# Optimization experiments

Hardware: AMD Instinct MI355X
Metric: run time of the kernel (lower is better)

Reference implementation:

```python
import jax, jax.numpy as jnp
import numpy as np

N_NODES = 25000
N_EDGES = 400000
N_GRAPHS = 100
D_IN = 16
D = 32          # node_dim
K = 11          # spectral coefficients = edge_dim
NOUT1 = 30
NOUT2 = 2
L = 2           # n_interactions
D_OUT = 32


def setup_inputs() -> dict:
    key = jax.random.key(0)
    ks = jax.random.split(key, 24)
    s = 0.1
    inp = {
        'x': jax.random.normal(ks[0], (N_NODES, D_IN), jnp.float32),
        'edge_attr': jax.random.uniform(ks[1], (N_EDGES, K), jnp.float32),
        'edge_index': jax.random.randint(ks[2], (2, N_EDGES), 0, N_NODES),
        'batch': jnp.sort(jax.random.randint(ks[3], (N_NODES,), 0, N_GRAPHS)),
        # embedding
        'emb_w': jax.random.normal(ks[4], (D_IN, D)) * s,
        'emb_b': jnp.zeros((D,)),
        # per-interaction params, stacked on leading L axis
        'init_w': jax.random.normal(ks[5], (L, D, D)) * s,             # initial_dense (no bias)
        'e1_w': jax.random.normal(ks[6], (L, K, 2 * K)) * s,
        'e2_w': jax.random.normal(ks[7], (L, K, 2 * K)) * s,
        'e3_w': jax.random.normal(ks[8], (L, K, 2 * K)) * s,
        'e4_w': jax.random.normal(ks[9], (L, 4 * K, K)) * s,
        'conv_w': jax.random.normal(ks[10], (L, K, D, NOUT1)) * s,     # SpectConv weight (selfconn=False)
        'conv_b': jnp.zeros((L, NOUT1)),
        'att_v': jax.random.normal(ks[11], (L, D, 1)) * s,
        'skip1_w': jax.random.normal(ks[12], (L, D, NOUT2)) * s,
        'skip1_b': jnp.full((L, NOUT2), 0.01),
        'skip2_w': jax.random.normal(ks[13], (L, D, NOUT2)) * s,
        'skip2_b': jnp.full((L, NOUT2), 0.01),
        'out_w': jax.random.normal(ks[14], (L, NOUT1 + NOUT2, D)) * s,
        'out_b': jnp.full((L, D), 0.01),
        # encoder output head
        'final_w': jax.random.normal(ks[15], (D, D_OUT)) * s,
        'final_b': jnp.zeros((D_OUT,)),
    }
    return inp


def _segment_softmax(raw, dst, n):
    m = jax.ops.segment_max(raw, dst, num_segments=n)
    m = jnp.where(jnp.isfinite(m), m, 0.0)
    e = jnp.exp(raw - m[dst])
    denom = jax.ops.segment_sum(e, dst, num_segments=n)
    return e / (denom[dst] + 1e-16)


def _interaction(h, src, dst, edge_attr, p):
    (init_w, e1_w, e2_w, e3_w, e4_w, conv_w, conv_b, att_v,
     s1_w, s1_b, s2_w, s2_b, out_w, out_b) = p
    n = h.shape[0]
    h_proj = h @ init_w                                     # [N, D]
    # learned edge transform
    lin = jax.nn.relu(edge_attr @ e1_w)                     # [E, 2K]
    gate = jnp.tanh(edge_attr @ e2_w) * jnp.tanh(edge_attr @ e3_w)
    ea = jax.nn.relu(jnp.concatenate([lin, gate], axis=1) @ e4_w)  # [E, K]
    # spectral conv with attention (selfconn=False)
    xs = h_proj[src]                                        # gather [E, D]
    msgs = ea[:, :, None] * xs[:, None, :]                  # [E, K, D]
    agg = jax.ops.segment_sum(msgs, dst, num_segments=n)    # [N, K, D]
    sum_out = jnp.einsum('nkd,kdo->no', agg, conv_w)        # [N, NOUT1]
    pooled = ea.mean(axis=1, keepdims=True) * xs            # mean_k msg_k, [E, D]
    raw_att = (pooled @ att_v)[:, 0]                        # [E]
    att = _segment_softmax(raw_att, dst, n)                 # [E]
    att_agg = jax.ops.segment_sum(att[:, None, None] * msgs, dst, num_segments=n)
    att_out = jnp.einsum('nkd,kdo->no', att_agg, conv_w)
    conv_out = jax.nn.relu(sum_out + att_out + conv_b)      # [N, NOUT1]
    skip = jnp.tanh(h_proj @ s1_w + s1_b) * jnp.tanh(h_proj @ s2_w + s2_b)  # [N, NOUT2]
    layer_out = jnp.concatenate([conv_out, skip], axis=1)
    delta = layer_out @ out_w + out_b                       # [N, D]
    return delta, att


def reference(x, edge_attr, emb_w, emb_b, init_w, e1_w, e2_w, e3_w, e4_w,
              conv_w, conv_b, att_v, skip1_w, skip1_b, skip2_w, skip2_b,
              out_w, out_b, final_w, final_b, edge_index, batch):
    src, dst = edge_index[0], edge_index[1]
    h = x @ emb_w + emb_b                                   # node embedding [N, D]
    atts = []
    for l in range(L):
        p = (init_w[l], e1_w[l], e2_w[l], e3_w[l], e4_w[l], conv_w[l], conv_b[l],
             att_v[l], skip1_w[l], skip1_b[l], skip2_w[l], skip2_b[l], out_w[l], out_b[l])
        delta, att = _interaction(h, src, dst, edge_attr, p)
        h = h + delta                                       # residual
        atts.append(att)
    # global mean pool per graph
    counts = jax.ops.segment_sum(jnp.ones((h.shape[0],), h.dtype), batch, num_segments=N_GRAPHS)
    pooled = jax.ops.segment_sum(h, batch, num_segments=N_GRAPHS) / jnp.maximum(counts, 1.0)[:, None]
    output = pooled @ final_w + final_b                     # [G, D_OUT]
    return output, h, jnp.stack(atts)
```

## Files before the change

### kernel.cpp

```cpp
#include <hip/hip_runtime.h>
#include <hip/hip_bf16.h>

typedef __hip_bfloat16 bf16;
using f32x4v = __attribute__((ext_vector_type(4))) float;
using bf16x8 = __attribute__((ext_vector_type(8))) short;

#define N_NODES 25000
#define N_PAD   25024
#define N_EDGES 400000
#define N_GR    100
#define SCAN_C  25

__device__ __forceinline__ bf16 tob(float v) { return __float2bfloat16(v); }
__device__ __forceinline__ unsigned short tobu(float v) {
  union { bf16 b; unsigned short u; } c; c.b = __float2bfloat16(v); return c.u;
}
__device__ __forceinline__ float b2f(unsigned short u) { return __uint_as_float(((unsigned)u) << 16); }
__device__ __forceinline__ float tanh_fast(float x) {
  float e = __expf(2.f * x);
  return 1.f - 2.f * __builtin_amdgcn_rcpf(e + 1.f);
}

__global__ __launch_bounds__(256) void hist_kernel(const int* __restrict__ dst, int* __restrict__ deg, int E) {
  int e = blockIdx.x * blockDim.x + threadIdx.x;
  if (e < E) atomicAdd(&deg[dst[e]], 1);
}

__global__ __launch_bounds__(1024) void scan_kernel(const int* __restrict__ deg, int* __restrict__ offs,
                                                    int* __restrict__ cur, int n) {
  __shared__ int wsum[16];
  __shared__ int wpre[16];
  int t = threadIdx.x, lane = t & 63, w = t >> 6;
  int base = t * SCAN_C;
  int loc[SCAN_C];
  int s = 0;
  #pragma unroll
  for (int i = 0; i < SCAN_C; i++) {
    int idx = base + i;
    int v = (idx < n) ? deg[idx] : 0;
    loc[i] = s; s += v;
  }
  int x = s;
  #pragma unroll
  for (int sh = 1; sh < 64; sh <<= 1) { int y = __shfl_up(x, sh); if (lane >= sh) x += y; }
  if (lane == 63) wsum[w] = x;
  __syncthreads();
  if (w == 0 && lane < 16) {
    int ws_ = wsum[lane], xs = ws_;
    #pragma unroll
    for (int sh = 1; sh < 16; sh <<= 1) { int y = __shfl_up(xs, sh); if (lane >= sh) xs += y; }
    wpre[lane] = xs - ws_;
  }
  __syncthreads();
  int excl = wpre[w] + x - s;
  #pragma unroll
  for (int i = 0; i < SCAN_C; i++) {
    int idx = base + i;
    if (idx < n) { int o = excl + loc[i]; offs[idx] = o; cur[idx] = o; }
  }
  if (t == 1023) offs[n] = excl + s;
}

__global__ __launch_bounds__(256) void prep_kernel(const float* __restrict__ e1, const float* __restrict__ e2,
                                                   const float* __restrict__ e3, const float* __restrict__ e4,
                                                   const float* __restrict__ attv, const float* __restrict__ convw,
                                                   const float* __restrict__ outw,
                                                   const int* __restrict__ batch,
                                                   float* __restrict__ wE, bf16* __restrict__ Wt,
                                                   bf16* __restrict__ owB, int* __restrict__ gb,
                                                   int* __restrict__ deg) {
  int i = blockIdx.x * blockDim.x + threadIdx.x;
  if (i < N_NODES) deg[i] = 0;
  if (i < 2 * 1352) {
    int l = i / 1352, r = i % 1352;
    float v = 0.f;
    if (r < 264)       { int q = r;        int j = q / 12, k = q % 12; if (k < 11) v = e1[l*242 + k*22 + j]; }
    else if (r < 528)  { int q = r - 264;  int j = q / 12, k = q % 12; if (k < 11) v = e2[l*242 + k*22 + j]; }
    else if (r < 792)  { int q = r - 528;  int j = q / 12, k = q % 12; if (k < 11) v = e3[l*242 + k*22 + j]; }
    else if (r < 1056) { int q = r - 792;  int j = q / 12, k = q % 12; if (k < 11) v = e4[l*484 + j*11 + k]; }
    else if (r < 1320) { int q = r - 1056; int j = q / 12, k = q % 12; if (k < 11) v = e4[l*484 + (22 + j)*11 + k]; }
    else               { int d = r - 1320; v = attv[l*32 + d]; }
    wE[i] = v;
  }
  int t = i - 2 * 1352;
  if (t >= 0 && t < 2 * 32 * 352) {
    int l = t / (32 * 352), q = t % (32 * 352);
    int o = q / 352, dk = q % 352;
    int d = dk / 11, kk = dk % 11;
    float v = 0.f;
    if (o < 30) v = convw[l*10560 + (kk*32 + d)*30 + o];
    Wt[t] = tob(v);
  }
  int u = i - 2 * 1352 - 2 * 32 * 352;
  if (u >= 0 && u < 2048) {
    int l = u >> 10, rem = u & 1023;
    int hf = rem >> 9, rem2 = rem & 511;
    int lane = rem2 >> 3, j = rem2 & 7;
    int k = (lane >> 4) * 8 + j, n = lane & 15;
    owB[u] = tob(outw[l*1024 + k*32 + hf*16 + n]);
  }
  int g = i - 2 * 1352 - 2 * 32 * 352 - 2048;
  if (g >= 0 && g <= N_GR) {
    if (g == N_GR) { gb[g] = N_NODES; }
    else {
      int lo = 0, hi = N_NODES;
      while (lo < hi) { int mid = (lo + hi) >> 1; if (batch[mid] < g) lo = mid + 1; else hi = mid; }
      gb[g] = lo;
    }
  }
}

__global__ __launch_bounds__(256) void emb_hproj_kernel(const float* __restrict__ x, const float* __restrict__ w,
                                                        const float* __restrict__ b, const float* __restrict__ w1,
                                                        float* __restrict__ h, float* __restrict__ hp,
                                                        unsigned short* __restrict__ hpb, int N) {
  __shared__ float semb[16 * 32];
  __shared__ float sw1[32 * 32];
  __shared__ float sb[32];
  __shared__ float sx[8][16];
  __shared__ float sh[8][33];
  int tid = threadIdx.x;
  for (int i = tid; i < 16 * 32; i += 256) semb[i] = w[i];
  for (int i = tid; i < 32 * 32; i += 256) sw1[i] = w1[i];
  if (tid < 32) sb[tid] = b[tid];
  int nb = blockIdx.x * 8;
  if (tid < 128) {
    int n = nb + (tid >> 4), k = tid & 15;
    sx[tid >> 4][k] = (n < N) ? x[(size_t)n * 16 + k] : 0.f;
  }
  __syncthreads();
  int grp = tid >> 5, d = tid & 31;
  int n = nb + grp;
  float acc = sb[d];
  #pragma unroll
  for (int k = 0; k < 16; k++) acc += sx[grp][k] * semb[k*32 + d];
  sh[grp][d] = acc;
  if (n < N) h[(size_t)n * 32 + d] = acc;
  __syncthreads();
  float hpv = 0.f;
  #pragma unroll
  for (int k = 0; k < 32; k++) hpv += sh[grp][k] * sw1[k*32 + d];
  if (n < N) {
    hp[(size_t)n * 32 + d] = hpv;
    hpb[(size_t)n * 32 + d] = tobu(hpv);
  }
}

__device__ __forceinline__ void loadw12(const float4* base, int idx3, float* w) {
  float4 a = base[idx3], b = base[idx3 + 1], c = base[idx3 + 2];
  w[0]=a.x; w[1]=a.y; w[2]=a.z; w[3]=a.w;
  w[4]=b.x; w[5]=b.y; w[6]=b.z; w[7]=b.w;
  w[8]=c.x; w[9]=c.y; w[10]=c.z; w[11]=c.w;
}

__global__ __launch_bounds__(256) void edge_mlp_kernel(const float* __restrict__ eattr,
                                                       const int* __restrict__ srcA,
                                                       const int* __restrict__ dstA,
                                                       int* __restrict__ cur,
                                                       int* __restrict__ elist,
                                                       const float* __restrict__ wE0,
                                                       const float* __restrict__ wE1,
                                                       uint4* __restrict__ pay0,
                                                       uint4* __restrict__ pay1, int E) {
  const float4* wa = (const float4*)wE0;
  const float4* wb = (const float4*)wE1;
  int e = blockIdx.x * blockDim.x + threadIdx.x;
  bool live = e < E;
  float a[11], acc0[11], acc1[11];
  #pragma unroll
  for (int k = 0; k < 11; k++) {
    a[k] = live ? eattr[(size_t)e*11 + k] : 0.f;
    acc0[k] = 0.f; acc1[k] = 0.f;
  }
  int pp = 0, s = 0;
  if (live) {
    s = srcA[e];
    pp = atomicAdd(&cur[dstA[e]], 1);
    elist[pp] = e;
  }
  for (int j = 0; j < 22; j++) {
    float wA[12], wB[12], wC[12];
    loadw12(wa, j*3, wA);
    loadw12(wa, 66 + j*3, wB);
    loadw12(wa, 132 + j*3, wC);
    float l1a = 0.f, l2a = 0.f, l3a = 0.f;
    #pragma unroll
    for (int k = 0; k < 11; k++) { l1a += a[k]*wA[k]; l2a += a[k]*wB[k]; l3a += a[k]*wC[k]; }
    loadw12(wb, j*3, wA);
    loadw12(wb, 66 + j*3, wB);
    loadw12(wb, 132 + j*3, wC);
    float l1b = 0.f, l2b = 0.f, l3b = 0.f;
    #pragma unroll
    for (int k = 0; k < 11; k++) { l1b += a[k]*wA[k]; l2b += a[k]*wB[k]; l3b += a[k]*wC[k]; }
    float gga = tanh_fast(l2a) * tanh_fast(l3a);
    float ggb = tanh_fast(l2b) * tanh_fast(l3b);
    l1a = fmaxf(l1a, 0.f);
    l1b = fmaxf(l1b, 0.f);
    loadw12(wa, 198 + j*3, wA);
    loadw12(wa, 264 + j*3, wB);
    #pragma unroll
    for (int k = 0; k < 11; k++) acc0[k] += l1a*wA[k] + gga*wB[k];
    loadw12(wb, 198 + j*3, wA);
    loadw12(wb, 264 + j*3, wB);
    #pragma unroll
    for (int k = 0; k < 11; k++) acc1[k] += l1b*wA[k] + ggb*wB[k];
  }
  if (!live) return;
  float mean0 = 0.f, mean1 = 0.f;
  #pragma unroll
  for (int k = 0; k < 11; k++) {
    acc0[k] = fmaxf(acc0[k], 0.f); mean0 += acc0[k];
    acc1[k] = fmaxf(acc1[k], 0.f); mean1 += acc1[k];
  }
  mean0 *= (1.f / 11.f);
  mean1 *= (1.f / 11.f);
  unsigned q[6];
  #pragma unroll
  for (int m = 0; m < 5; m++)
    q[m] = (unsigned)tobu(acc0[2*m]) | ((unsigned)tobu(acc0[2*m+1]) << 16);
  q[5] = (unsigned)tobu(acc0[10]);
  pay0[(size_t)pp * 2]     = make_uint4(q[0], q[1], q[2], q[3]);
  pay0[(size_t)pp * 2 + 1] = make_uint4(q[4], q[5], __float_as_uint(mean0), (unsigned)s);
  #pragma unroll
  for (int m = 0; m < 5; m++)
    q[m] = (unsigned)tobu(acc1[2*m]) | ((unsigned)tobu(acc1[2*m+1]) << 16);
  q[5] = (unsigned)tobu(acc1[10]);
  pay1[(size_t)pp * 2]     = make_uint4(q[0], q[1], q[2], q[3]);
  pay1[(size_t)pp * 2 + 1] = make_uint4(q[4], q[5], __float_as_uint(mean1), (unsigned)s);
}

__global__ __launch_bounds__(256) void edge_raw_kernel(uint4* __restrict__ pay,
                                                       const unsigned short* __restrict__ hpb,
                                                       const float* __restrict__ attvl, int E) {
  int p = blockIdx.x * blockDim.x + threadIdx.x;
  if (p >= E) return;
  uint4 m1 = pay[(size_t)p * 2 + 1];
  float mean = __uint_as_float(m1.z);
  int s = (int)m1.w;
  const uint2* hb = (const uint2*)(hpb + (size_t)s * 32);
  float dot = 0.f;
  #pragma unroll
  for (int q = 0; q < 8; q++) {
    uint2 hv = hb[q];
    dot += b2f((unsigned short)hv.x) * attvl[q*4+0] + b2f((unsigned short)(hv.x >> 16)) * attvl[q*4+1]
         + b2f((unsigned short)hv.y) * attvl[q*4+2] + b2f((unsigned short)(hv.y >> 16)) * attvl[q*4+3];
  }
  ((float*)pay)[(size_t)p * 8 + 6] = mean * dot;
}

__device__ __forceinline__ void unpack_pay(uint4 p0, uint4 p1, float* ev) {
  ev[0] = b2f((unsigned short)p0.x); ev[1] = b2f((unsigned short)(p0.x >> 16));
  ev[2] = b2f((unsigned short)p0.y); ev[3] = b2f((unsigned short)(p0.y >> 16));
  ev[4] = b2f((unsigned short)p0.z); ev[5] = b2f((unsigned short)(p0.z >> 16));
  ev[6] = b2f((unsigned short)p0.w); ev[7] = b2f((unsigned short)(p0.w >> 16));
  ev[8] = b2f((unsigned short)p1.x); ev[9] = b2f((unsigned short)(p1.x >> 16));
  ev[10] = b2f((unsigned short)p1.y);
}

__global__ __launch_bounds__(256) void node_kernel(const int* __restrict__ offs, const int* __restrict__ elist,
                                                   const uint4* __restrict__ pay,
                                                   const unsigned short* __restrict__ hpb,
                                                   bf16* __restrict__ Abuf, float* __restrict__ atts, int N) {
  int wid = threadIdx.x >> 6, lane = threadIdx.x & 63;
  int half = lane >> 5, d = lane & 31;
  int n = blockIdx.x * 4 + wid;
  if (n >= N_PAD) return;
  int beg = 0, deg = 0;
  if (n < N) { beg = offs[n]; deg = offs[n + 1] - beg; }
  const float* payf = (const float*)pay;

  float M, inv;
  float einv_reg = 0.f;
  bool fast = (deg <= 64);
  if (fast) {
    float r = (lane < deg) ? payf[(size_t)(beg + lane) * 8 + 6] : -1e30f;
    float mm = r;
    #pragma unroll
    for (int sh = 1; sh < 64; sh <<= 1) mm = fmaxf(mm, __shfl_xor(mm, sh));
    M = mm;
    float ex = (lane < deg) ? __expf(r - M) : 0.f;
    float ss = ex;
    #pragma unroll
    for (int sh = 1; sh < 64; sh <<= 1) ss += __shfl_xor(ss, sh);
    inv = 1.f / (ss + 1e-16f);
    einv_reg = ex * inv;
    if (lane < deg) atts[elist[beg + lane]] = einv_reg;
  } else {
    float m_l = -1e30f;
    for (int jj = lane; jj < deg; jj += 64)
      m_l = fmaxf(m_l, payf[(size_t)(beg + jj) * 8 + 6]);
    #pragma unroll
    for (int sh = 1; sh < 64; sh <<= 1) m_l = fmaxf(m_l, __shfl_xor(m_l, sh));
    M = m_l;
    float s_l = 0.f;
    for (int jj = lane; jj < deg; jj += 64)
      s_l += __expf(payf[(size_t)(beg + jj) * 8 + 6] - M);
    #pragma unroll
    for (int sh = 1; sh < 64; sh <<= 1) s_l += __shfl_xor(s_l, sh);
    inv = 1.f / (s_l + 1e-16f);
    for (int jj = lane; jj < deg; jj += 64) {
      float r = payf[(size_t)(beg + jj) * 8 + 6];
      atts[elist[beg + jj]] = __expf(r - M) * inv;
    }
  }

  float agg[11];
  #pragma unroll
  for (int k = 0; k < 11; k++) agg[k] = 0.f;

  int j = half;
  for (; j + 2 < deg; j += 4) {
    uint4 a0 = pay[(size_t)(beg + j) * 2],     a1 = pay[(size_t)(beg + j) * 2 + 1];
    uint4 b0 = pay[(size_t)(beg + j + 2) * 2], b1 = pay[(size_t)(beg + j + 2) * 2 + 1];
    float xa = b2f(hpb[(size_t)(int)a1.w * 32 + d]);
    float xb = b2f(hpb[(size_t)(int)b1.w * 32 + d]);
    float ca = fast ? (1.f + __shfl(einv_reg, j))
                    : (1.f + __expf(__uint_as_float(a1.z) - M) * inv);
    float cb = fast ? (1.f + __shfl(einv_reg, j + 2))
                    : (1.f + __expf(__uint_as_float(b1.z) - M) * inv);
    float cxa = ca * xa, cxb = cb * xb;
    float eva[11], evb[11];
    unpack_pay(a0, a1, eva);
    unpack_pay(b0, b1, evb);
    #pragma unroll
    for (int k = 0; k < 11; k++) agg[k] += eva[k] * cxa + evb[k] * cxb;
  }
  for (; j < deg; j += 2) {
    uint4 q0 = pay[(size_t)(beg + j) * 2], q1 = pay[(size_t)(beg + j) * 2 + 1];
    float xs = b2f(hpb[(size_t)(int)q1.w * 32 + d]);
    float c = fast ? (1.f + __shfl(einv_reg, j))
                   : (1.f + __expf(__uint_as_float(q1.z) - M) * inv);
    float cx = c * xs;
    float ev[11];
    unpack_pay(q0, q1, ev);
    #pragma unroll
    for (int k = 0; k < 11; k++) agg[k] += ev[k] * cx;
  }

  #pragma unroll
  for (int k = 0; k < 11; k++) agg[k] += __shfl_xor(agg[k], 32);

  if (half == 0) {
    bf16* arow = Abuf + (size_t)n * 352 + d * 11;
    #pragma unroll
    for (int k = 0; k < 11; k++) arow[k] = tob(agg[k]);
  }
}

__global__ __launch_bounds__(128) void convfused_kernel(const short* __restrict__ A, const short* __restrict__ Wt,
                                                        const short* __restrict__ owB,
                                                        const float* __restrict__ hp, float* __restrict__ h,
                                                        const float* __restrict__ convb,
                                                        const float* __restrict__ s1w, const float* __restrict__ s1b,
                                                        const float* __restrict__ s2w, const float* __restrict__ s2b,
                                                        const float* __restrict__ outb,
                                                        const float* __restrict__ initw_next,
                                                        float* __restrict__ hp_out, unsigned short* __restrict__ hpb_out,
                                                        int N) {
  __shared__ short slo[32][40];
  __shared__ float sdelta[32][36];
  __shared__ float sskipw[128];
  __shared__ float sskipb[4];
  __shared__ float scb[32];
  __shared__ float sob[32];
  __shared__ float sw1[1024];
  int tid = threadIdx.x;
  if (tid < 64) sskipw[tid] = s1w[tid];
  if (tid >= 64 && tid < 128) sskipw[tid] = s2w[tid - 64];
  if (tid < 32) sob[tid] = outb[tid];
  if (tid >= 32 && tid < 64) scb[tid - 32] = (tid - 32 < 30) ? convb[tid - 32] : 0.f;
  if (tid >= 96 && tid < 100) sskipb[tid - 96] = (tid < 98) ? s1b[tid - 96] : s2b[tid - 98];
  if (initw_next) {
    for (int i = tid; i < 1024; i += 128) sw1[i] = initw_next[i];
  }
  __syncthreads();

  int wave = tid >> 6, lane = tid & 63;
  int r16 = lane & 15, kq = lane >> 4;
  int mbase = blockIdx.x * 32 + wave * 16;

  const short* arow = A + (size_t)(mbase + r16) * 352 + kq * 8;
  const short* b0p = Wt + (size_t)r16 * 352 + kq * 8;
  const short* b1p = b0p + 16 * 352;
  f32x4v acc0 = {0.f, 0.f, 0.f, 0.f}, acc1 = {0.f, 0.f, 0.f, 0.f};
  #pragma unroll
  for (int ks = 0; ks < 11; ks++) {
    bf16x8 af = *(const bf16x8*)(arow + ks * 32);
    bf16x8 b0 = *(const bf16x8*)(b0p + ks * 32);
    bf16x8 b1 = *(const bf16x8*)(b1p + ks * 32);
    acc0 = __builtin_amdgcn_mfma_f32_16x16x32_bf16(af, b0, acc0, 0, 0, 0);
    acc1 = __builtin_amdgcn_mfma_f32_16x16x32_bf16(af, b1, acc1, 0, 0, 0);
  }
  #pragma unroll
  for (int r = 0; r < 4; r++) {
    int row = wave * 16 + kq * 4 + r;
    slo[row][r16] = (short)tobu(fmaxf(acc0[r] + scb[r16], 0.f));
    if (r16 < 14) slo[row][16 + r16] = (short)tobu(fmaxf(acc1[r] + scb[16 + r16], 0.f));
  }
  __syncthreads();

  if (tid < 64) {
    int row = tid >> 1, jx = tid & 1;
    int grow = blockIdx.x * 32 + row;
    float a1 = sskipb[jx], a2 = sskipb[2 + jx];
    if (grow < N) {
      const float* hr = hp + (size_t)grow * 32;
      #pragma unroll
      for (int dd = 0; dd < 32; dd++) {
        float hv = hr[dd];
        a1 += hv * sskipw[dd*2 + jx];
        a2 += hv * sskipw[64 + dd*2 + jx];
      }
    }
    slo[row][30 + jx] = (short)tobu(tanh_fast(a1) * tanh_fast(a2));
  }
  __syncthreads();

  bf16x8 a2f = *(const bf16x8*)&slo[wave * 16 + r16][kq * 8];
  bf16x8 bo0 = *(const bf16x8*)(owB + lane * 8);
  bf16x8 bo1 = *(const bf16x8*)(owB + 512 + lane * 8);
  f32x4v d0 = {0.f, 0.f, 0.f, 0.f}, d1 = {0.f, 0.f, 0.f, 0.f};
  d0 = __builtin_amdgcn_mfma_f32_16x16x32_bf16(a2f, bo0, d0, 0, 0, 0);
  d1 = __builtin_amdgcn_mfma_f32_16x16x32_bf16(a2f, bo1, d1, 0, 0, 0);
  #pragma unroll
  for (int r = 0; r < 4; r++) {
    int row = wave * 16 + kq * 4 + r;
    sdelta[row][r16] = d0[r] + sob[r16];
    sdelta[row][16 + r16] = d1[r] + sob[16 + r16];
  }
  __syncthreads();

  int row = tid >> 2, col0 = (tid & 3) * 8;
  int grow = blockIdx.x * 32 + row;
  if (grow < N) {
    float* hr = h + (size_t)grow * 32 + col0;
    float4 ha = *(float4*)hr;
    float4 hb = *(float4*)(hr + 4);
    float4 da = *(float4*)&sdelta[row][col0];
    float4 db = *(float4*)&sdelta[row][col0 + 4];
    ha.x += da.x; ha.y += da.y; ha.z += da.z; ha.w += da.w;
    hb.x += db.x; hb.y += db.y; hb.z += db.z; hb.w += db.w;
    *(float4*)hr = ha;
    *(float4*)(hr + 4) = hb;
    *(float4*)&sdelta[row][col0] = ha;
    *(float4*)&sdelta[row][col0 + 4] = hb;
  }
  if (initw_next) {
    __syncthreads();
    if (grow < N) {
      float o[8];
      #pragma unroll
      for (int c = 0; c < 8; c++) o[c] = 0.f;
      #pragma unroll
      for (int k = 0; k < 32; k++) {
        float hv = sdelta[row][k];
        #pragma unroll
        for (int c = 0; c < 8; c++) o[c] += hv * sw1[k*32 + col0 + c];
      }
      float* hpo = hp_out + (size_t)grow * 32 + col0;
      unsigned short* hbo = hpb_out + (size_t)grow * 32 + col0;
      #pragma unroll
      for (int c = 0; c < 8; c++) { hpo[c] = o[c]; hbo[c] = tobu(o[c]); }
    }
  }
}

__global__ __launch_bounds__(256) void pool2_kernel(const float* __restrict__ h, const int* __restrict__ gb,
                                                    const float* __restrict__ fw, const float* __restrict__ fb,
                                                    float* __restrict__ out0, float* __restrict__ outh) {
  __shared__ float part[8][32];
  __shared__ float pooled[32];
  int g = blockIdx.x;
  int s = gb[g], e = gb[g + 1];
  int grp = threadIdx.x >> 5, d = threadIdx.x & 31;
  float acc = 0.f;
  for (int n = s + grp; n < e; n += 8) {
    float v = h[(size_t)n * 32 + d];
    outh[(size_t)n * 32 + d] = v;
    acc += v;
  }
  part[grp][d] = acc;
  __syncthreads();
  if (threadIdx.x < 32) {
    float sum = 0.f;
    #pragma unroll
    for (int i = 0; i < 8; i++) sum += part[i][d];
    pooled[d] = sum / fmaxf((float)(e - s), 1.f);
  }
  __syncthreads();
  if (threadIdx.x < 32) {
    int jx = threadIdx.x;
    float o = fb[jx];
    #pragma unroll
    for (int dd = 0; dd < 32; dd++) o += pooled[dd] * fw[dd*32 + jx];
    out0[g * 32 + jx] = o;
  }
}

extern "C" void kernel_launch(void* const* d_in, const int* in_sizes, int n_in,
                              void* d_out, int out_size, void* d_ws, size_t ws_size,
                              hipStream_t stream) {
  (void)in_sizes; (void)n_in; (void)out_size; (void)ws_size;
  const float* x      = (const float*)d_in[0];
  const float* eattr  = (const float*)d_in[1];
  const int* eidx     = (const int*)d_in[2];
  const int* batch    = (const int*)d_in[3];
  const float* emb_w  = (const float*)d_in[4];
  const float* emb_b  = (const float*)d_in[5];
  const float* init_w = (const float*)d_in[6];
  const float* e1w    = (const float*)d_in[7];
  const float* e2w    = (const float*)d_in[8];
  const float* e3w    = (const float*)d_in[9];
  const float* e4w    = (const float*)d_in[10];
  const float* convw  = (const float*)d_in[11];
  const float* convb  = (const float*)d_in[12];
  const float* attv   = (const float*)d_in[13];
  const float* s1w    = (const float*)d_in[14];
  const float* s1b    = (const float*)d_in[15];
  const float* s2w    = (const float*)d_in[16];
  const float* s2b    = (const float*)d_in[17];
  const float* outw   = (const float*)d_in[18];
  const float* outb   = (const float*)d_in[19];
  const float* finw   = (const float*)d_in[20];
  const float* finb   = (const float*)d_in[21];

  char* ws = (char*)d_ws;
  size_t off = 0;
  auto take = [&](size_t bytes) -> char* {
    char* p = ws + off;
    off += (bytes + 255) & ~(size_t)255;
    return p;
  };
  float* h    = (float*)take((size_t)N_NODES * 32 * 4);
  float* hp   = (float*)take((size_t)N_NODES * 32 * 4);
  unsigned short* hpb = (unsigned short*)take((size_t)N_NODES * 32 * 2);
  uint4* pay0 = (uint4*)take((size_t)N_EDGES * 32);
  uint4* pay1 = (uint4*)take((size_t)N_EDGES * 32);
  bf16*  Abuf = (bf16*)take((size_t)N_PAD * 352 * 2);
  int*   deg  = (int*)take((size_t)N_NODES * 4);
  int*   offs = (int*)take((size_t)(N_NODES + 1) * 4);
  int*   cur  = (int*)take((size_t)N_NODES * 4);
  int*   elist= (int*)take((size_t)N_EDGES * 4);
  int*   gb   = (int*)take((size_t)(N_GR + 1) * 4);
  float* wE   = (float*)take((size_t)2 * 1352 * 4);
  bf16*  Wt   = (bf16*)take((size_t)2 * 32 * 352 * 2);
  bf16*  owB  = (bf16*)take((size_t)2048 * 2);

  float* out0 = (float*)d_out;
  float* outh = out0 + N_GR * 32;
  float* outa = outh + (size_t)N_NODES * 32;

  const int* srcA = eidx;
  const int* dstA = eidx + N_EDGES;

  prep_kernel<<<107, 256, 0, stream>>>(e1w, e2w, e3w, e4w, attv, convw, outw, batch, wE, Wt, owB, gb, deg);
  hist_kernel<<<(N_EDGES + 255) / 256, 256, 0, stream>>>(dstA, deg, N_EDGES);
  scan_kernel<<<1, 1024, 0, stream>>>(deg, offs, cur, N_NODES);
  edge_mlp_kernel<<<(N_EDGES + 255) / 256, 256, 0, stream>>>(
      eattr, srcA, dstA, cur, elist, wE, wE + 1352, pay0, pay1, N_EDGES);
  emb_hproj_kernel<<<(N_NODES + 7) / 8, 256, 0, stream>>>(x, emb_w, emb_b, init_w, h, hp, hpb, N_NODES);

  for (int l = 0; l < 2; l++) {
    uint4* pay = (l == 0) ? pay0 : pay1;
    edge_raw_kernel<<<(N_EDGES + 255) / 256, 256, 0, stream>>>(
        pay, hpb, wE + l * 1352 + 1320, N_EDGES);
    node_kernel<<<N_PAD / 4, 256, 0, stream>>>(offs, elist, pay, hpb,
                                               Abuf, outa + (size_t)l * N_EDGES, N_NODES);
    convfused_kernel<<<N_PAD / 32, 128, 0, stream>>>(
        (const short*)Abuf, (const short*)Wt + (size_t)l * 32 * 352, (const short*)owB + (size_t)l * 1024,
        hp, h, convb + l * 30, s1w + l * 64, s1b + l * 2, s2w + l * 64, s2b + l * 2,
        outb + l * 32,
        (l == 0) ? (init_w + 1024) : nullptr, hp, hpb, N_NODES);
  }

  pool2_kernel<<<N_GR, 256, 0, stream>>>(h, gb, finw, finb, out0, outh);
}
```

Before: 241.5 us.

## Split CSR fill from edge MLP and interleave per-layer edge payloads

Moves the CSR fill (atomic slot claim and elist write) into its own kernel, so the edge MLP runs in CSR order. It reads edge attributes by gathering through elist and writes both layers' payloads contiguously into one 64-byte record. The attention logits go to a separate dense rawv array instead of being patched into the payload. The intent is fully coalesced payload stores and a contiguous logit read in the node kernel. In exchange it adds a kernel launch, scattered edge-attribute reads, and a strided 32-byte read per layer from the combined record.

```diff
diff --git a/kernel.cpp b/kernel.cpp
--- a/kernel.cpp
+++ b/kernel.cpp
@@ -59,6 +59,12 @@
     if (idx < n) { int o = excl + loc[i]; offs[idx] = o; cur[idx] = o; }
   }
   if (t == 1023) offs[n] = excl + s;
+}
+
+__global__ __launch_bounds__(256) void fill_kernel(const int* __restrict__ dstA, int* __restrict__ cur,
+                                                   int* __restrict__ elist, int E) {
+  int e = blockIdx.x * blockDim.x + threadIdx.x;
+  if (e < E) { int p = atomicAdd(&cur[dstA[e]], 1); elist[p] = e; }
 }
 
 __global__ __launch_bounds__(256) void prep_kernel(const float* __restrict__ e1, const float* __restrict__ e2,
@@ -155,28 +161,21 @@
 
 __global__ __launch_bounds__(256) void edge_mlp_kernel(const float* __restrict__ eattr,
                                                        const int* __restrict__ srcA,
-                                                       const int* __restrict__ dstA,
-                                                       int* __restrict__ cur,
-                                                       int* __restrict__ elist,
+                                                       const int* __restrict__ elist,
                                                        const float* __restrict__ wE0,
                                                        const float* __restrict__ wE1,
-                                                       uint4* __restrict__ pay0,
-                                                       uint4* __restrict__ pay1, int E) {
+                                                       uint4* __restrict__ payC, int E) {
   const float4* wa = (const float4*)wE0;
   const float4* wb = (const float4*)wE1;
-  int e = blockIdx.x * blockDim.x + threadIdx.x;
-  bool live = e < E;
+  int p = blockIdx.x * blockDim.x + threadIdx.x;
+  bool live = p < E;
+  int e = live ? elist[p] : 0;
+  int s = live ? srcA[e] : 0;
   float a[11], acc0[11], acc1[11];
   #pragma unroll
   for (int k = 0; k < 11; k++) {
     a[k] = live ? eattr[(size_t)e*11 + k] : 0.f;
     acc0[k] = 0.f; acc1[k] = 0.f;
-  }
-  int pp = 0, s = 0;
-  if (live) {
-    s = srcA[e];
-    pp = atomicAdd(&cur[dstA[e]], 1);
-    elist[pp] = e;
   }
   for (int j = 0; j < 22; j++) {
     float wA[12], wB[12], wC[12];
@@ -214,29 +213,30 @@
   }
   mean0 *= (1.f / 11.f);
   mean1 *= (1.f / 11.f);
-  unsigned q[6];
-  #pragma unroll
-  for (int m = 0; m < 5; m++)
-    q[m] = (unsigned)tobu(acc0[2*m]) | ((unsigned)tobu(acc0[2*m+1]) << 16);
-  q[5] = (unsigned)tobu(acc0[10]);
-  pay0[(size_t)pp * 2]     = make_uint4(q[0], q[1], q[2], q[3]);
-  pay0[(size_t)pp * 2 + 1] = make_uint4(q[4], q[5], __float_as_uint(mean0), (unsigned)s);
-  #pragma unroll
-  for (int m = 0; m < 5; m++)
-    q[m] = (unsigned)tobu(acc1[2*m]) | ((unsigned)tobu(acc1[2*m+1]) << 16);
-  q[5] = (unsigned)tobu(acc1[10]);
-  pay1[(size_t)pp * 2]     = make_uint4(q[0], q[1], q[2], q[3]);
-  pay1[(size_t)pp * 2 + 1] = make_uint4(q[4], q[5], __float_as_uint(mean1), (unsigned)s);
-}
-
-__global__ __launch_bounds__(256) void edge_raw_kernel(uint4* __restrict__ pay,
+  unsigned q0[6], q1[6];
+  #pragma unroll
+  for (int m = 0; m < 5; m++) {
+    q0[m] = (unsigned)tobu(acc0[2*m]) | ((unsigned)tobu(acc0[2*m+1]) << 16);
+    q1[m] = (unsigned)tobu(acc1[2*m]) | ((unsigned)tobu(acc1[2*m+1]) << 16);
+  }
+  q0[5] = (unsigned)tobu(acc0[10]);
+  q1[5] = (unsigned)tobu(acc1[10]);
+  uint4* rec = payC + (size_t)p * 4;
+  rec[0] = make_uint4(q0[0], q0[1], q0[2], q0[3]);
+  rec[1] = make_uint4(q0[4], q0[5], __float_as_uint(mean0), (unsigned)s);
+  rec[2] = make_uint4(q1[0], q1[1], q1[2], q1[3]);
+  rec[3] = make_uint4(q1[4], q1[5], __float_as_uint(mean1), (unsigned)s);
+}
+
+__global__ __launch_bounds__(256) void edge_raw_kernel(const uint4* __restrict__ payC, int lay,
                                                        const unsigned short* __restrict__ hpb,
-                                                       const float* __restrict__ attvl, int E) {
+                                                       const float* __restrict__ attvl,
+                                                       float* __restrict__ rawv, int E) {
   int p = blockIdx.x * blockDim.x + threadIdx.x;
   if (p >= E) return;
-  uint4 m1 = pay[(size_t)p * 2 + 1];
-  float mean = __uint_as_float(m1.z);
-  int s = (int)m1.w;
+  uint4 meta = payC[(size_t)p * 4 + lay * 2 + 1];
+  float mean = __uint_as_float(meta.z);
+  int s = (int)meta.w;
   const uint2* hb = (const uint2*)(hpb + (size_t)s * 32);
   float dot = 0.f;
   #pragma unroll
@@ -245,7 +245,7 @@
     dot += b2f((unsigned short)hv.x) * attvl[q*4+0] + b2f((unsigned short)(hv.x >> 16)) * attvl[q*4+1]
          + b2f((unsigned short)hv.y) * attvl[q*4+2] + b2f((unsigned short)(hv.y >> 16)) * attvl[q*4+3];
   }
-  ((float*)pay)[(size_t)p * 8 + 6] = mean * dot;
+  rawv[p] = mean * dot;
 }
 
 __device__ __forceinline__ void unpack_pay(uint4 p0, uint4 p1, float* ev) {
@@ -258,7 +258,8 @@
 }
 
 __global__ __launch_bounds__(256) void node_kernel(const int* __restrict__ offs, const int* __restrict__ elist,
-                                                   const uint4* __restrict__ pay,
+                                                   const uint4* __restrict__ payC, int lay,
+                                                   const float* __restrict__ rawv,
                                                    const unsigned short* __restrict__ hpb,
                                                    bf16* __restrict__ Abuf, float* __restrict__ atts, int N) {
   int wid = threadIdx.x >> 6, lane = threadIdx.x & 63;
@@ -267,13 +268,13 @@
   if (n >= N_PAD) return;
   int beg = 0, deg = 0;
   if (n < N) { beg = offs[n]; deg = offs[n + 1] - beg; }
-  const float* payf = (const float*)pay;
+  int off2 = lay * 2;
 
   float M, inv;
   float einv_reg = 0.f;
   bool fast = (deg <= 64);
   if (fast) {
-    float r = (lane < deg) ? payf[(size_t)(beg + lane) * 8 + 6] : -1e30f;
+    float r = (lane < deg) ? rawv[beg + lane] : -1e30f;
     float mm = r;
     #pragma unroll
     for (int sh = 1; sh < 64; sh <<= 1) mm = fmaxf(mm, __shfl_xor(mm, sh));
@@ -288,20 +289,18 @@
   } else {
     float m_l = -1e30f;
     for (int jj = lane; jj < deg; jj += 64)
-      m_l = fmaxf(m_l, payf[(size_t)(beg + jj) * 8 + 6]);
+      m_l = fmaxf(m_l, rawv[beg + jj]);
     #pragma unroll
     for (int sh = 1; sh < 64; sh <<= 1) m_l = fmaxf(m_l, __shfl_xor(m_l, sh));
     M = m_l;
     float s_l = 0.f;
     for (int jj = lane; jj < deg; jj += 64)
-      s_l += __expf(payf[(size_t)(beg + jj) * 8 + 6] - M);
+      s_l += __expf(rawv[beg + jj] - M);
     #pragma unroll
     for (int sh = 1; sh < 64; sh <<= 1) s_l += __shfl_xor(s_l, sh);
     inv = 1.f / (s_l + 1e-16f);
-    for (int jj = lane; jj < deg; jj += 64) {
-      float r = payf[(size_t)(beg + jj) * 8 + 6];
-      atts[elist[beg + jj]] = __expf(r - M) * inv;
-    }
+    for (int jj = lane; jj < deg; jj += 64)
+      atts[elist[beg + jj]] = __expf(rawv[beg + jj] - M) * inv;
   }
 
   float agg[11];
@@ -310,14 +309,14 @@
 
   int j = half;
   for (; j + 2 < deg; j += 4) {
-    uint4 a0 = pay[(size_t)(beg + j) * 2],     a1 = pay[(size_t)(beg + j) * 2 + 1];
-    uint4 b0 = pay[(size_t)(beg + j + 2) * 2], b1 = pay[(size_t)(beg + j + 2) * 2 + 1];
+    uint4 a0 = payC[(size_t)(beg + j) * 4 + off2],     a1 = payC[(size_t)(beg + j) * 4 + off2 + 1];
+    uint4 b0 = payC[(size_t)(beg + j + 2) * 4 + off2], b1 = payC[(size_t)(beg + j + 2) * 4 + off2 + 1];
     float xa = b2f(hpb[(size_t)(int)a1.w * 32 + d]);
     float xb = b2f(hpb[(size_t)(int)b1.w * 32 + d]);
     float ca = fast ? (1.f + __shfl(einv_reg, j))
-                    : (1.f + __expf(__uint_as_float(a1.z) - M) * inv);
+                    : (1.f + __expf(rawv[beg + j] - M) * inv);
     float cb = fast ? (1.f + __shfl(einv_reg, j + 2))
-                    : (1.f + __expf(__uint_as_float(b1.z) - M) * inv);
+                    : (1.f + __expf(rawv[beg + j + 2] - M) * inv);
     float cxa = ca * xa, cxb = cb * xb;
     float eva[11], evb[11];
     unpack_pay(a0, a1, eva);
@@ -326,10 +325,10 @@
     for (int k = 0; k < 11; k++) agg[k] += eva[k] * cxa + evb[k] * cxb;
   }
   for (; j < deg; j += 2) {
-    uint4 q0 = pay[(size_t)(beg + j) * 2], q1 = pay[(size_t)(beg + j) * 2 + 1];
+    uint4 q0 = payC[(size_t)(beg + j) * 4 + off2], q1 = payC[(size_t)(beg + j) * 4 + off2 + 1];
     float xs = b2f(hpb[(size_t)(int)q1.w * 32 + d]);
     float c = fast ? (1.f + __shfl(einv_reg, j))
-                   : (1.f + __expf(__uint_as_float(q1.z) - M) * inv);
+                   : (1.f + __expf(rawv[beg + j] - M) * inv);
     float cx = c * xs;
     float ev[11];
     unpack_pay(q0, q1, ev);
@@ -534,8 +533,8 @@
   float* h    = (float*)take((size_t)N_NODES * 32 * 4);
   float* hp   = (float*)take((size_t)N_NODES * 32 * 4);
   unsigned short* hpb = (unsigned short*)take((size_t)N_NODES * 32 * 2);
-  uint4* pay0 = (uint4*)take((size_t)N_EDGES * 32);
-  uint4* pay1 = (uint4*)take((size_t)N_EDGES * 32);
+  uint4* payC = (uint4*)take((size_t)N_EDGES * 64);
+  float* rawv = (float*)take((size_t)N_EDGES * 4);
   bf16*  Abuf = (bf16*)take((size_t)N_PAD * 352 * 2);
   int*   deg  = (int*)take((size_t)N_NODES * 4);
   int*   offs = (int*)take((size_t)(N_NODES + 1) * 4);
@@ -556,15 +555,15 @@
   prep_kernel<<<107, 256, 0, stream>>>(e1w, e2w, e3w, e4w, attv, convw, outw, batch, wE, Wt, owB, gb, deg);
   hist_kernel<<<(N_EDGES + 255) / 256, 256, 0, stream>>>(dstA, deg, N_EDGES);
   scan_kernel<<<1, 1024, 0, stream>>>(deg, offs, cur, N_NODES);
+  fill_kernel<<<(N_EDGES + 255) / 256, 256, 0, stream>>>(dstA, cur, elist, N_EDGES);
   edge_mlp_kernel<<<(N_EDGES + 255) / 256, 256, 0, stream>>>(
-      eattr, srcA, dstA, cur, elist, wE, wE + 1352, pay0, pay1, N_EDGES);
+      eattr, srcA, elist, wE, wE + 1352, payC, N_EDGES);
   emb_hproj_kernel<<<(N_NODES + 7) / 8, 256, 0, stream>>>(x, emb_w, emb_b, init_w, h, hp, hpb, N_NODES);
 
   for (int l = 0; l < 2; l++) {
-    uint4* pay = (l == 0) ? pay0 : pay1;
     edge_raw_kernel<<<(N_EDGES + 255) / 256, 256, 0, stream>>>(
-        pay, hpb, wE + l * 1352 + 1320, N_EDGES);
-    node_kernel<<<N_PAD / 4, 256, 0, stream>>>(offs, elist, pay, hpb,
+        payC, l, hpb, wE + l * 1352 + 1320, rawv, N_EDGES);
+    node_kernel<<<N_PAD / 4, 256, 0, stream>>>(offs, elist, payC, l, rawv, hpb,
                                                Abuf, outa + (size_t)l * N_EDGES, N_NODES);
     convfused_kernel<<<N_PAD / 32, 128, 0, stream>>>(
         (const short*)Abuf, (const short*)Wt + (size_t)l * 32 * 352, (const short*)owB + (size_t)l * 1024,
```

Result: slower. 263.9 us (+9.3%).
